# Kernel tuning notes

Hardware: AMD Instinct MI355X
Metric: run time of the kernel (lower is better)

The kernel has to match this reference:

```python
import jax, jax.numpy as jnp
import numpy as np

B, N, D, M, DEPTH, VOCAB = 8, 128, 128, 16, 4, 100
EIN = 2 * D + 1          # edge MLP input dim: feats_i | feats_j | rel_dist
LN_EPS = 1e-5


def setup_inputs() -> dict:
    key = jax.random.key(0)
    ks = jax.random.split(key, 20)
    s = 0.02  # small init like egnn-pytorch's init_eps
    f32 = jnp.float32
    return {
        "z": jax.random.randint(ks[0], (B, N), 0, VOCAB),
        "pos": jax.random.normal(ks[1], (B, N, 3), f32),
        "mask": jnp.ones((B, N), bool),
        "emb": jax.random.normal(ks[2], (VOCAB, D), f32) * s,
        # edge MLP: Linear(EIN, 2*EIN) -> SiLU -> Linear(2*EIN, M) -> SiLU
        "e_w1": jax.random.normal(ks[3], (DEPTH, EIN, 2 * EIN), f32) * s,
        "e_b1": jnp.zeros((DEPTH, 2 * EIN), f32),
        "e_w2": jax.random.normal(ks[4], (DEPTH, 2 * EIN, M), f32) * s,
        "e_b2": jnp.zeros((DEPTH, M), f32),
        # coors MLP: Linear(M, 4M) -> SiLU -> Linear(4M, 1)
        "c_w1": jax.random.normal(ks[5], (DEPTH, M, 4 * M), f32) * s,
        "c_b1": jnp.zeros((DEPTH, 4 * M), f32),
        "c_w2": jax.random.normal(ks[6], (DEPTH, 4 * M, 1), f32) * s,
        "c_b2": jnp.zeros((DEPTH, 1), f32),
        # node LayerNorm (norm_feats=True in EGNN_Network)
        "ln_g": jnp.ones((DEPTH, D), f32),
        "ln_b": jnp.zeros((DEPTH, D), f32),
        # node MLP: Linear(D+M, 2D) -> SiLU -> Linear(2D, D), residual
        "n_w1": jax.random.normal(ks[7], (DEPTH, D + M, 2 * D), f32) * s,
        "n_b1": jnp.zeros((DEPTH, 2 * D), f32),
        "n_w2": jax.random.normal(ks[8], (DEPTH, 2 * D, D), f32) * s,
        "n_b2": jnp.zeros((DEPTH, D), f32),
    }


def _egnn_forward(z, pos, mask, emb, e_w1, e_b1, e_w2, e_b2,
                  c_w1, c_b1, c_w2, c_b2, ln_g, ln_b,
                  n_w1, n_b1, n_w2, n_b2):
    feats = emb[z]                       # [B,N,D]
    coors = pos                          # [B,N,3]
    mf = mask.astype(feats.dtype)        # [B,N]
    pair = mf[:, :, None] * mf[:, None, :]   # [B,N,N] pairwise mask
    for l in range(DEPTH):
        rel = coors[:, :, None, :] - coors[:, None, :, :]       # [B,N,N,3]
        dist = jnp.sum(rel * rel, axis=-1, keepdims=True)       # [B,N,N,1]
        fi = jnp.broadcast_to(feats[:, :, None, :], (B, N, N, D))
        fj = jnp.broadcast_to(feats[:, None, :, :], (B, N, N, D))
        e = jnp.concatenate([fi, fj, dist], axis=-1)             # [B,N,N,EIN]
        h = jax.nn.silu(e @ e_w1[l] + e_b1[l])                   # [B,N,N,2*EIN]
        m_ij = jax.nn.silu(h @ e_w2[l] + e_b2[l])                # [B,N,N,M]
        # coordinate update
        cw = (jax.nn.silu(m_ij @ c_w1[l] + c_b1[l]) @ c_w2[l] + c_b2[l])[..., 0]
        cw = cw * pair                                           # mask invalid pairs
        coors = coors + jnp.einsum('bij,bijc->bic', cw, rel)
        # node update: masked sum-pool of messages over j
        m_i = jnp.sum(m_ij * pair[..., None], axis=2)            # [B,N,M]
        mu = jnp.mean(feats, axis=-1, keepdims=True)
        var = jnp.var(feats, axis=-1, keepdims=True)
        fn = (feats - mu) * jax.lax.rsqrt(var + LN_EPS) * ln_g[l] + ln_b[l]
        ni = jnp.concatenate([fn, m_i], axis=-1)                 # [B,N,D+M]
        feats = feats + (jax.nn.silu(ni @ n_w1[l] + n_b1[l]) @ n_w2[l] + n_b2[l])
    # masked mean pool
    w = mf[..., None]
    return jnp.sum(feats * w, axis=1) / jnp.maximum(jnp.sum(w, axis=1), 1.0)


def reference(z, pos, mask, emb, e_w1, e_b1, e_w2, e_b2,
              c_w1, c_b1, c_w2, c_b2, ln_g, ln_b,
              n_w1, n_b1, n_w2, n_b2):
    return _egnn_forward(z, pos, mask, emb, e_w1, e_b1, e_w2, e_b2,
                         c_w1, c_b1, c_w2, c_b2, ln_g, ln_b,
                         n_w1, n_b1, n_w2, n_b2)
```

## Files before the change

### kernel.cpp

```cpp
#include <hip/hip_runtime.h>

#define BATCH 8
#define NN    128
#define DD    128
#define MM    16
#define DEPTH 4
#define EIN   257
#define H1    514
#define KPAD  544
#define NCH   17
#define NODES (BATCH*NN)
#define BQ_B  69632
#define NL2E  (-1.442695040888963f)
#define NLN2  (-0.6931471805599453f)

typedef __attribute__((ext_vector_type(8))) short short8;
typedef __attribute__((ext_vector_type(4))) float floatx4;

__device__ __forceinline__ float b2f(unsigned short u) {
    return __uint_as_float(((unsigned int)u) << 16);
}
__device__ __forceinline__ unsigned short f2b(float f) {
    unsigned int x = __float_as_uint(f);
    unsigned int r = (x + 0x7fffu + ((x >> 16) & 1u)) >> 16;
    return (unsigned short)r;
}
__device__ __forceinline__ float siluf(float x) {
    float t = __builtin_amdgcn_exp2f(x * NL2E);
    return x * __builtin_amdgcn_rcpf(1.0f + t);
}
__device__ __forceinline__ float loadf(const void* p, size_t idx, int isbf) {
    return isbf ? b2f(((const unsigned short*)p)[idx]) : ((const float*)p)[idx];
}
__device__ __forceinline__ unsigned int pk2(float x, float y) {
    unsigned int xb = __float_as_uint(x) + 0x8000u;
    unsigned int yb = __float_as_uint(y) + 0x8000u;
    return __builtin_amdgcn_perm(yb, xb, 0x07060302);
}
__device__ __forceinline__ unsigned int h2pk_y(float y0, float y1) {
    float t0 = __builtin_amdgcn_exp2f(y0);
    float t1 = __builtin_amdgcn_exp2f(y1);
    float h0 = y0 * __builtin_amdgcn_rcpf(1.0f + t0);
    float h1 = y1 * __builtin_amdgcn_rcpf(1.0f + t1);
    return pk2(h0, h1);
}

#define OFF_FEATS   0
#define OFF_COORSA  131072
#define OFF_COORSB  134144
#define OFF_AB      137216
#define OFF_BQ      694272
#define OFF_CPK     1267712
#define OFF_WLB     1272576
#define OFF_W2F     1274816
#define OFF_FLAG    1292224
#define OFF_FB16    1292228
#define OFF_W1F     1357764

__global__ __launch_bounds__(256) void k_init(
    const int* __restrict__ z, const void* __restrict__ pos,
    const void* __restrict__ emb,
    const void* __restrict__ e_w1, const void* __restrict__ e_w2,
    const void* __restrict__ e_b2,
    const void* __restrict__ c_w1, const void* __restrict__ c_b1,
    const void* __restrict__ c_w2, const void* __restrict__ c_b2,
    float* __restrict__ feats, unsigned short* __restrict__ fb16,
    float* __restrict__ coorsA,
    float* __restrict__ wlb, int4* __restrict__ w2frag,
    int4* __restrict__ w1frag,
    float* __restrict__ cpack, int* __restrict__ flag) {
    __shared__ int sfl;
    int tid = threadIdx.x, bx = blockIdx.x;
    if (tid < 64) {
        float f = fabsf(__uint_as_float(((const unsigned int*)pos)[tid]));
        bool ok = (f == 0.f) || (f > 1e-8f && f < 1e8f);
        unsigned long long v = __ballot(ok);
        if (tid == 0) sfl = (__builtin_popcountll(v) >= 32) ? 0 : 1;
    }
    __syncthreads();
    int isbf = sfl;
    if (bx == 0 && tid == 0) *flag = isbf;
    if (bx < 512) {
        int node = 2 * bx + (tid >> 7), t = tid & 127;
        int zi = z[node];
        float v = loadf(emb, (size_t)zi * DD + t, isbf);
        feats[node * DD + t] = v;
        fb16[node * DD + t] = f2b(v);
        if (t < 3) coorsA[node * 3 + t] = loadf(pos, node * 3 + t, isbf);
    } else if (bx < 580) {
        int p = bx - 512;
        int layer = p / NCH, kc = p % NCH;
        if (tid < 64) {
            int quad = tid >> 4, c = tid & 15;
            size_t w2base = (size_t)layer * H1 * MM;
            unsigned int u[4];
            #pragma unroll
            for (int pp = 0; pp < 4; ++pp) {
                int k0 = kc * 32 + quad * 8 + 2 * pp, k1 = k0 + 1;
                float f0 = (k0 < H1) ? loadf(e_w2, w2base + (size_t)k0 * MM + c, isbf) : 0.f;
                float f1 = (k1 < H1) ? loadf(e_w2, w2base + (size_t)k1 * MM + c, isbf) : 0.f;
                u[pp] = pk2(f0, f1);
            }
            w2frag[(layer * NCH + kc) * 64 + tid] =
                make_int4((int)u[0], (int)u[1], (int)u[2], (int)u[3]);
            if (kc == 0) {
                size_t wlbase = ((size_t)layer * EIN + 256) * H1;
                for (int t = tid; t < KPAD; t += 64)
                    wlb[layer * 560 + t] =
                        (t < H1) ? NL2E * loadf(e_w1, wlbase + t, isbf) : 0.f;
                if (tid < 16)
                    wlb[layer * 560 + 544 + tid] = loadf(e_b2, layer * MM + tid, isbf);
            }
        }
    } else if (bx < 584) {
        int l = bx - 580;
        for (int idx = tid; idx < 1024; idx += 256) {
            int c = idx >> 6, hh = idx & 63;
            cpack[l * 1216 + hh * 16 + c] = loadf(c_w1, l * 1024 + c * 64 + hh, isbf);
        }
        if (tid < 64)        cpack[l * 1216 + 1024 + tid] = loadf(c_b1, l * 64 + tid, isbf);
        else if (tid < 128)  cpack[l * 1216 + 1088 + tid - 64] = loadf(c_w2, l * 64 + tid - 64, isbf);
        else if (tid == 128) cpack[l * 1216 + 1152] = loadf(c_b2, l, isbf);
    } else {
        int p = bx - 584;
        int l = p / 68, nt = p % 68;
        int kcd = tid >> 6, lane = tid & 63;
        int quad = lane >> 4, c16 = lane & 15;
        int n_local = nt * 16 + c16;
        int half = n_local >= KPAD;
        int k_out = n_local - (half ? KPAD : 0);
        size_t wbase = (size_t)l * EIN * H1 + (size_t)(half ? 128 : 0) * H1 + k_out;
        unsigned int u[4];
        #pragma unroll
        for (int pp = 0; pp < 4; ++pp) {
            int d0 = kcd * 32 + quad * 8 + 2 * pp;
            float f0 = (k_out < H1) ? loadf(e_w1, wbase + (size_t)d0 * H1, isbf) : 0.f;
            float f1 = (k_out < H1) ? loadf(e_w1, wbase + (size_t)(d0 + 1) * H1, isbf) : 0.f;
            u[pp] = pk2(f0, f1);
        }
        w1frag[((size_t)(l * 68 + nt) * 4 + kcd) * 64 + lane] =
            make_int4((int)u[0], (int)u[1], (int)u[2], (int)u[3]);
    }
}

__global__ __launch_bounds__(256) void k1_ab(
    const unsigned short* __restrict__ fb16, const int4* __restrict__ w1f,
    const void* __restrict__ b1raw, unsigned int b1off,
    float* __restrict__ Ab, float* __restrict__ Bq,
    const int* __restrict__ flagp) {
    int bx = blockIdx.x;
    int mt = bx & 63, ng = bx >> 6;
    int tid = threadIdx.x, w = tid >> 6, lane = tid & 63;
    int quad = lane >> 4, c16 = lane & 15;
    int isbf = *flagp;
    int ntile = ng * 4 + w;
    int n_local = ntile * 16 + c16;
    int half = n_local >= KPAD;
    int k_out = n_local - (half ? KPAD : 0);

    const unsigned short* ap = fb16 + (size_t)(mt * 16 + c16) * DD + quad * 8;
    const int4* bp = w1f + (size_t)ntile * 4 * 64 + lane;
    floatx4 acc = {0.f, 0.f, 0.f, 0.f};
    #pragma unroll
    for (int kcd = 0; kcd < 4; ++kcd) {
        short8 af = *(const short8*)(ap + kcd * 32);
        union { int4 i4; short8 s; } bf;
        bf.i4 = bp[kcd * 64];
        acc = __builtin_amdgcn_mfma_f32_16x16x32_bf16(af, bf.s, acc, 0, 0, 0);
    }
    if (!half) {
        float bias = (k_out < H1) ? loadf(b1raw, b1off + k_out, isbf) : 0.f;
        #pragma unroll
        for (int r = 0; r < 4; ++r)
            Ab[(size_t)(mt * 16 + quad * 4 + r) * KPAD + k_out] =
                NL2E * (acc[r] + bias);
    } else {
        int kc = k_out >> 5, kk = k_out & 31;
        int qd = kk >> 3, hsel = (kk >> 2) & 1, tt = k_out & 3;
        #pragma unroll
        for (int r = 0; r < 4; ++r) {
            int node = mt * 16 + quad * 4 + r;
            int bb = node >> 7, j = node & 127;
            int jt = j >> 4, lj = qd * 16 + (j & 15);
            Bq[(size_t)bb * BQ_B + kc * 4096 + jt * 512 + hsel * 256
               + lj * 4 + tt] = NL2E * acc[r];
        }
    }
}

#define K2_CHUNK(kc_) {                                                       \
    short8 bf = wfp[(kc_) * 64];                                              \
    float4 aA0 = *(const float4*)(arow0 + (kc_) * 32);                        \
    float4 aA1 = *(const float4*)(arow0 + (kc_) * 32 + 4);                    \
    float4 aB0 = *(const float4*)(arow1 + (kc_) * 32);                        \
    float4 aB1 = *(const float4*)(arow1 + (kc_) * 32 + 4);                    \
    float4 l0  = *(const float4*)(wlr + (kc_) * 32);                          \
    float4 l1  = *(const float4*)(wlr + (kc_) * 32 + 4);                      \
    float4 pp0 = *(const float4*)(bqw + (size_t)(kc_) * 4096);                \
    float4 pp1 = *(const float4*)(bqw + (size_t)(kc_) * 4096 + 256);          \
    float4 qq0 = *(const float4*)(bqw + (size_t)(kc_) * 4096 + 2048);         \
    float4 qq1 = *(const float4*)(bqw + (size_t)(kc_) * 4096 + 2304);         \
    union { unsigned int u[4]; short8 s; } ua, ub, uc, ud;                    \
    ua.u[0] = h2pk_y(fmaf(d2a0, l0.x, aA0.x + pp0.x),                         \
                     fmaf(d2a0, l0.y, aA0.y + pp0.y));                        \
    ua.u[1] = h2pk_y(fmaf(d2a0, l0.z, aA0.z + pp0.z),                         \
                     fmaf(d2a0, l0.w, aA0.w + pp0.w));                        \
    ua.u[2] = h2pk_y(fmaf(d2a0, l1.x, aA1.x + pp1.x),                         \
                     fmaf(d2a0, l1.y, aA1.y + pp1.y));                        \
    ua.u[3] = h2pk_y(fmaf(d2a0, l1.z, aA1.z + pp1.z),                         \
                     fmaf(d2a0, l1.w, aA1.w + pp1.w));                        \
    ub.u[0] = h2pk_y(fmaf(d2b0, l0.x, aA0.x + qq0.x),                         \
                     fmaf(d2b0, l0.y, aA0.y + qq0.y));                        \
    ub.u[1] = h2pk_y(fmaf(d2b0, l0.z, aA0.z + qq0.z),                         \
                     fmaf(d2b0, l0.w, aA0.w + qq0.w));                        \
    ub.u[2] = h2pk_y(fmaf(d2b0, l1.x, aA1.x + qq1.x),                         \
                     fmaf(d2b0, l1.y, aA1.y + qq1.y));                        \
    ub.u[3] = h2pk_y(fmaf(d2b0, l1.z, aA1.z + qq1.z),                         \
                     fmaf(d2b0, l1.w, aA1.w + qq1.w));                        \
    uc.u[0] = h2pk_y(fmaf(d2a1, l0.x, aB0.x + pp0.x),                         \
                     fmaf(d2a1, l0.y, aB0.y + pp0.y));                        \
    uc.u[1] = h2pk_y(fmaf(d2a1, l0.z, aB0.z + pp0.z),                         \
                     fmaf(d2a1, l0.w, aB0.w + pp0.w));                        \
    uc.u[2] = h2pk_y(fmaf(d2a1, l1.x, aB1.x + pp1.x),                         \
                     fmaf(d2a1, l1.y, aB1.y + pp1.y));                        \
    uc.u[3] = h2pk_y(fmaf(d2a1, l1.z, aB1.z + pp1.z),                         \
                     fmaf(d2a1, l1.w, aB1.w + pp1.w));                        \
    ud.u[0] = h2pk_y(fmaf(d2b1, l0.x, aB0.x + qq0.x),                         \
                     fmaf(d2b1, l0.y, aB0.y + qq0.y));                        \
    ud.u[1] = h2pk_y(fmaf(d2b1, l0.z, aB0.z + qq0.z),                         \
                     fmaf(d2b1, l0.w, aB0.w + qq0.w));                        \
    ud.u[2] = h2pk_y(fmaf(d2b1, l1.x, aB1.x + qq1.x),                         \
                     fmaf(d2b1, l1.y, aB1.y + qq1.y));                        \
    ud.u[3] = h2pk_y(fmaf(d2b1, l1.z, aB1.z + qq1.z),                         \
                     fmaf(d2b1, l1.w, aB1.w + qq1.w));                        \
    acc00 = __builtin_amdgcn_mfma_f32_16x16x32_bf16(ua.s, bf, acc00, 0, 0, 0);\
    acc01 = __builtin_amdgcn_mfma_f32_16x16x32_bf16(ub.s, bf, acc01, 0, 0, 0);\
    acc10 = __builtin_amdgcn_mfma_f32_16x16x32_bf16(uc.s, bf, acc10, 0, 0, 0);\
    acc11 = __builtin_amdgcn_mfma_f32_16x16x32_bf16(ud.s, bf, acc11, 0, 0, 0);}

__global__ __launch_bounds__(512, 4) void k2_pair(
    const float* __restrict__ Ab, const float* __restrict__ Bq,
    const float* __restrict__ coorsIn, float* __restrict__ coorsOut,
    float* __restrict__ feats, unsigned short* __restrict__ fb16,
    const float* __restrict__ wlbL,
    const short8* __restrict__ w2fragL,
    const float* __restrict__ cpk,
    const void* __restrict__ gln, const void* __restrict__ bln,
    const void* __restrict__ w1r, const void* __restrict__ b1r,
    const void* __restrict__ w2r, const void* __restrict__ b2r,
    unsigned int layer, const int* __restrict__ flagp) {
    __shared__ float Ms[2][128 * 17];
    __shared__ float px[128], py[128], pz[128];
    __shared__ float msum[2][16][16];
    __shared__ float cwf[2][2][128];
    __shared__ float red[4][3];
    __shared__ float fr[2][128];
    __shared__ float ni[2][144];
    __shared__ float hid[2][256];
    __shared__ float part[2][2][128];
    int tid = threadIdx.x;
    int b = blockIdx.x & 7, ip = blockIdx.x >> 3;
    int i0 = ip * 2;
    int node0 = b * NN + i0;
    int w = tid >> 6, lane = tid & 63;
    int quad = lane >> 4, c16 = lane & 15;
    int kg = w >> 2, wj = w & 3;
    int isbf = *flagp;

    if (tid < 128) {
        int g = (b * NN + tid) * 3;
        px[tid] = coorsIn[g]; py[tid] = coorsIn[g + 1]; pz[tid] = coorsIn[g + 2];
    } else if (tid < 384) {
        int n = (tid - 128) >> 7, t = tid & 127;
        fr[n][t] = feats[(size_t)(node0 + n) * DD + t];
    }
    __syncthreads();

    int j0 = wj * 16 + c16, j1 = j0 + 64;
    float p0x = px[i0],     p0y = py[i0],     p0z = pz[i0];
    float p1x = px[i0 + 1], p1y = py[i0 + 1], p1z = pz[i0 + 1];
    float dxa0 = p0x - px[j0], dya0 = p0y - py[j0], dza0 = p0z - pz[j0];
    float d2a0 = dxa0*dxa0 + dya0*dya0 + dza0*dza0;
    float dxb0 = p0x - px[j1], dyb0 = p0y - py[j1], dzb0 = p0z - pz[j1];
    float d2b0 = dxb0*dxb0 + dyb0*dyb0 + dzb0*dzb0;
    float dxa1 = p1x - px[j0], dya1 = p1y - py[j0], dza1 = p1z - pz[j0];
    float d2a1 = dxa1*dxa1 + dya1*dya1 + dza1*dza1;
    float dxb1 = p1x - px[j1], dyb1 = p1y - py[j1], dzb1 = p1z - pz[j1];
    float d2b1 = dxb1*dxb1 + dyb1*dyb1 + dzb1*dzb1;
    float b2v = wlbL[544 + c16];

    const float* arow0 = Ab + (size_t)node0 * KPAD + quad * 8;
    const float* arow1 = arow0 + KPAD;
    const float* wlr   = wlbL + quad * 8;
    const float* bqw   = Bq + (size_t)b * BQ_B + wj * 512 + lane * 4;
    const short8* wfp  = w2fragL + lane;

    floatx4 acc00 = {0.f,0.f,0.f,0.f}, acc01 = {0.f,0.f,0.f,0.f};
    floatx4 acc10 = {0.f,0.f,0.f,0.f}, acc11 = {0.f,0.f,0.f,0.f};

    if (kg == 0) {
        K2_CHUNK(0) K2_CHUNK(1) K2_CHUNK(2) K2_CHUNK(3) K2_CHUNK(4)
        K2_CHUNK(5) K2_CHUNK(6) K2_CHUNK(7) K2_CHUNK(8)
    } else {
        K2_CHUNK(9) K2_CHUNK(10) K2_CHUNK(11) K2_CHUNK(12)
        K2_CHUNK(13) K2_CHUNK(14) K2_CHUNK(15) K2_CHUNK(16)
    }

    if (kg == 0) {
        #pragma unroll
        for (int r = 0; r < 4; ++r) {
            int jl = (wj * 16 + quad * 4 + r) * 17 + c16;
            Ms[0][jl]           = acc00[r];
            Ms[0][jl + 64 * 17] = acc01[r];
            Ms[1][jl]           = acc10[r];
            Ms[1][jl + 64 * 17] = acc11[r];
        }
    }
    __syncthreads();
    if (kg == 1) {
        #pragma unroll
        for (int r = 0; r < 4; ++r) {
            int jl = (wj * 16 + quad * 4 + r) * 17 + c16;
            Ms[0][jl]           = siluf(fmaf(Ms[0][jl]           + acc00[r], NLN2, b2v));
            Ms[0][jl + 64 * 17] = siluf(fmaf(Ms[0][jl + 64 * 17] + acc01[r], NLN2, b2v));
            Ms[1][jl]           = siluf(fmaf(Ms[1][jl]           + acc10[r], NLN2, b2v));
            Ms[1][jl + 64 * 17] = siluf(fmaf(Ms[1][jl + 64 * 17] + acc11[r], NLN2, b2v));
        }
    }
    __syncthreads();

    {
        int n = tid >> 8, g = (tid >> 4) & 15, c = tid & 15;
        float s = 0.f;
        #pragma unroll
        for (int t = 0; t < 8; ++t) s += Ms[n][(g * 8 + t) * 17 + c];
        msum[n][g][c] = s;
    }
    __syncthreads();

    if (tid < 32) {
        int n = tid >> 4, c = tid & 15;
        float s = 0.f;
        #pragma unroll
        for (int g = 0; g < 16; ++g) s += msum[n][g][c];
        ni[n][128 + c] = s;
    }
    if (tid < 128) {
        int n = tid >> 6; int l6 = tid & 63;
        unsigned int lnoff = layer * DD;
        float v0 = fr[n][l6], v1 = fr[n][l6 + 64];
        float s1 = v0 + v1, s2 = v0 * v0 + v1 * v1;
        #pragma unroll
        for (int off = 32; off >= 1; off >>= 1) {
            s1 += __shfl_xor(s1, off, 64);
            s2 += __shfl_xor(s2, off, 64);
        }
        float mu  = s1 * (1.0f / 128.0f);
        float var = s2 * (1.0f / 128.0f) - mu * mu;
        float rs  = rsqrtf(var + 1e-5f);
        ni[n][l6]      = (v0 - mu) * rs * loadf(gln, lnoff + l6, isbf)
                       + loadf(bln, lnoff + l6, isbf);
        ni[n][l6 + 64] = (v1 - mu) * rs * loadf(gln, lnoff + l6 + 64, isbf)
                       + loadf(bln, lnoff + l6 + 64, isbf);
    }

    {
        int n = tid >> 8, j = tid & 127, hf = (tid >> 7) & 1;
        float mv[16];
        #pragma unroll
        for (int c = 0; c < 16; ++c) mv[c] = Ms[n][j * 17 + c];
        float cwacc = hf ? 0.f : cpk[1152];
        #pragma unroll 2
        for (int hi = 0; hi < 32; ++hi) {
            int hh = (hf << 5) + hi;
            const float4* q = (const float4*)(cpk + hh * 16);
            float4 q0 = q[0], q1 = q[1], q2 = q[2], q3 = q[3];
            float t = cpk[1024 + hh]
                + mv[0]*q0.x + mv[1]*q0.y + mv[2]*q0.z + mv[3]*q0.w
                + mv[4]*q1.x + mv[5]*q1.y + mv[6]*q1.z + mv[7]*q1.w
                + mv[8]*q2.x + mv[9]*q2.y + mv[10]*q2.z + mv[11]*q2.w
                + mv[12]*q3.x + mv[13]*q3.y + mv[14]*q3.z + mv[15]*q3.w;
            cwacc += siluf(t) * cpk[1088 + hh];
        }
        cwf[n][hf][j] = cwacc;
    }
    __syncthreads();

    if (tid < 256) {
        int n = tid >> 7, j = tid & 127;
        float cw = cwf[n][0][j] + cwf[n][1][j];
        float pnx = (n == 0) ? p0x : p1x;
        float pny = (n == 0) ? p0y : p1y;
        float pnz = (n == 0) ? p0z : p1z;
        float vx = cw * (pnx - px[j]), vy = cw * (pny - py[j]),
              vz = cw * (pnz - pz[j]);
        #pragma unroll
        for (int off = 32; off >= 1; off >>= 1) {
            vx += __shfl_xor(vx, off, 64);
            vy += __shfl_xor(vy, off, 64);
            vz += __shfl_xor(vz, off, 64);
        }
        if (lane == 0) { red[w][0] = vx; red[w][1] = vy; red[w][2] = vz; }
    }

    {
        int n = tid >> 8, h = tid & 255;
        size_t w1off = (size_t)layer * 144 * 256;
        float acc = loadf(b1r, layer * 256 + h, isbf);
        if (isbf) {
            const unsigned short* wp = (const unsigned short*)w1r + w1off + h;
            #pragma unroll 8
            for (int d = 0; d < 144; ++d) acc += ni[n][d] * b2f(wp[(size_t)d * 256]);
        } else {
            const float* wp = (const float*)w1r + w1off + h;
            #pragma unroll 8
            for (int d = 0; d < 144; ++d) acc += ni[n][d] * wp[(size_t)d * 256];
        }
        hid[n][h] = siluf(acc);
    }
    __syncthreads();

    if (tid < 6) {
        int n = tid / 3, c = tid - n * 3;
        int nd = node0 + n;
        coorsOut[nd * 3 + c] = coorsIn[nd * 3 + c]
            + red[n * 2][c] + red[n * 2 + 1][c];
    }
    {
        int n = tid >> 8, d = tid & 127, hf = (tid >> 7) & 1;
        size_t w2off = (size_t)layer * 256 * 128;
        float acc = hf ? 0.f : loadf(b2r, layer * 128 + d, isbf);
        if (isbf) {
            const unsigned short* wp = (const unsigned short*)w2r + w2off
                                     + (size_t)hf * 128 * 128 + d;
            #pragma unroll 8
            for (int h = 0; h < 128; ++h) acc += hid[n][hf * 128 + h] * b2f(wp[(size_t)h * 128]);
        } else {
            const float* wp = (const float*)w2r + w2off + (size_t)hf * 128 * 128 + d;
            #pragma unroll 8
            for (int h = 0; h < 128; ++h) acc += hid[n][hf * 128 + h] * wp[(size_t)h * 128];
        }
        part[n][hf][d] = acc;
    }
    __syncthreads();
    if (tid < 256) {
        int n = tid >> 7, d = tid & 127;
        float v = fr[n][d] + part[n][0][d] + part[n][1][d];
        feats[(size_t)(node0 + n) * DD + d] = v;
        fb16[(size_t)(node0 + n) * DD + d] = f2b(v);
    }
}

__global__ __launch_bounds__(128) void k4_pool(
    const float* __restrict__ feats, void* __restrict__ out,
    const int* __restrict__ flagp) {
    int b = blockIdx.x, d = threadIdx.x;
    float s = 0.f;
    for (int n = 0; n < NN; ++n) s += feats[((size_t)(b * NN + n)) * DD + d];
    float v = s * (1.0f / 128.0f);
    if (*flagp) ((unsigned short*)out)[b * DD + d] = f2b(v);
    else        ((float*)out)[b * DD + d] = v;
}

extern "C" void kernel_launch(void* const* d_in, const int* in_sizes, int n_in,
                              void* d_out, int out_size, void* d_ws, size_t ws_size,
                              hipStream_t stream) {
    const int* z = (const int*)d_in[0];
    const void* pos  = d_in[1];
    const void* emb  = d_in[3];
    const void* e_w1 = d_in[4];
    const void* e_b1 = d_in[5];
    const void* e_w2 = d_in[6];
    const void* e_b2 = d_in[7];
    const void* c_w1 = d_in[8];
    const void* c_b1 = d_in[9];
    const void* c_w2 = d_in[10];
    const void* c_b2 = d_in[11];
    const void* ln_g = d_in[12];
    const void* ln_b = d_in[13];
    const void* n_w1 = d_in[14];
    const void* n_b1 = d_in[15];
    const void* n_w2 = d_in[16];
    const void* n_b2 = d_in[17];

    float* ws     = (float*)d_ws;
    float* feats  = ws + OFF_FEATS;
    float* coorsA = ws + OFF_COORSA;
    float* coorsB = ws + OFF_COORSB;
    float* Ab     = ws + OFF_AB;
    float* Bq     = ws + OFF_BQ;
    float* cpk    = ws + OFF_CPK;
    float* wlb    = ws + OFF_WLB;
    int4*  w2f    = (int4*)(ws + OFF_W2F);
    int*   flag   = (int*)(ws + OFF_FLAG);
    unsigned short* fb16 = (unsigned short*)(ws + OFF_FB16);
    int4*  w1f    = (int4*)(ws + OFF_W1F);

    k_init<<<856, 256, 0, stream>>>(
        z, pos, emb, e_w1, e_w2, e_b2, c_w1, c_b1, c_w2, c_b2,
        feats, fb16, coorsA, wlb, w2f, w1f, cpk, flag);

    float* cin = coorsA; float* cout = coorsB;
    for (int l = 0; l < DEPTH; ++l) {
        k1_ab<<<1088, 256, 0, stream>>>(
            fb16, w1f + (size_t)l * 68 * 4 * 64, e_b1,
            (unsigned int)(l * H1), Ab, Bq, flag);
        k2_pair<<<BATCH * NN / 2, 512, 0, stream>>>(
            Ab, Bq, cin, cout, feats, fb16,
            wlb + l * 560, (const short8*)(w2f + (size_t)l * NCH * 64),
            cpk + (size_t)l * 1216,
            ln_g, ln_b, n_w1, n_b1, n_w2, n_b2,
            (unsigned int)l, flag);
        float* t = cin; cin = cout; cout = t;
    }
    k4_pool<<<BATCH, 128, 0, stream>>>(feats, d_out, flag);
}
```

Measured before the change: 314.7 us.

## Process one node per block in pair kernel instead of two

The pair/node-update kernel now handles a single destination node per 512-thread block and launches one block per node, doubling the grid. The freed threads split the coordinate-MLP hidden loop, the node MLP first-layer reduction over inputs, and the second-layer reduction into more partial sums, which are combined in shared memory. The aim is more parallelism and occupancy, with fewer MFMA accumulators and registers per thread. In exchange, Bq tiles and node-MLP weights are reloaded once per node rather than shared across two nodes, which doubles that cache and memory traffic.

```diff
diff --git a/kernel.cpp b/kernel.cpp
--- a/kernel.cpp
+++ b/kernel.cpp
@@ -188,57 +188,37 @@
     }
 }
 
-#define K2_CHUNK(kc_) {                                                       \
+#define K2C(kc_) {                                                            \
     short8 bf = wfp[(kc_) * 64];                                              \
-    float4 aA0 = *(const float4*)(arow0 + (kc_) * 32);                        \
-    float4 aA1 = *(const float4*)(arow0 + (kc_) * 32 + 4);                    \
-    float4 aB0 = *(const float4*)(arow1 + (kc_) * 32);                        \
-    float4 aB1 = *(const float4*)(arow1 + (kc_) * 32 + 4);                    \
+    float4 aA0 = *(const float4*)(arow + (kc_) * 32);                         \
+    float4 aA1 = *(const float4*)(arow + (kc_) * 32 + 4);                     \
     float4 l0  = *(const float4*)(wlr + (kc_) * 32);                          \
     float4 l1  = *(const float4*)(wlr + (kc_) * 32 + 4);                      \
     float4 pp0 = *(const float4*)(bqw + (size_t)(kc_) * 4096);                \
     float4 pp1 = *(const float4*)(bqw + (size_t)(kc_) * 4096 + 256);          \
     float4 qq0 = *(const float4*)(bqw + (size_t)(kc_) * 4096 + 2048);         \
     float4 qq1 = *(const float4*)(bqw + (size_t)(kc_) * 4096 + 2304);         \
-    union { unsigned int u[4]; short8 s; } ua, ub, uc, ud;                    \
-    ua.u[0] = h2pk_y(fmaf(d2a0, l0.x, aA0.x + pp0.x),                         \
-                     fmaf(d2a0, l0.y, aA0.y + pp0.y));                        \
-    ua.u[1] = h2pk_y(fmaf(d2a0, l0.z, aA0.z + pp0.z),                         \
-                     fmaf(d2a0, l0.w, aA0.w + pp0.w));                        \
-    ua.u[2] = h2pk_y(fmaf(d2a0, l1.x, aA1.x + pp1.x),                         \
-                     fmaf(d2a0, l1.y, aA1.y + pp1.y));                        \
-    ua.u[3] = h2pk_y(fmaf(d2a0, l1.z, aA1.z + pp1.z),                         \
-                     fmaf(d2a0, l1.w, aA1.w + pp1.w));                        \
-    ub.u[0] = h2pk_y(fmaf(d2b0, l0.x, aA0.x + qq0.x),                         \
-                     fmaf(d2b0, l0.y, aA0.y + qq0.y));                        \
-    ub.u[1] = h2pk_y(fmaf(d2b0, l0.z, aA0.z + qq0.z),                         \
-                     fmaf(d2b0, l0.w, aA0.w + qq0.w));                        \
-    ub.u[2] = h2pk_y(fmaf(d2b0, l1.x, aA1.x + qq1.x),                         \
-                     fmaf(d2b0, l1.y, aA1.y + qq1.y));                        \
-    ub.u[3] = h2pk_y(fmaf(d2b0, l1.z, aA1.z + qq1.z),                         \
-                     fmaf(d2b0, l1.w, aA1.w + qq1.w));                        \
-    uc.u[0] = h2pk_y(fmaf(d2a1, l0.x, aB0.x + pp0.x),                         \
-                     fmaf(d2a1, l0.y, aB0.y + pp0.y));                        \
-    uc.u[1] = h2pk_y(fmaf(d2a1, l0.z, aB0.z + pp0.z),                         \
-                     fmaf(d2a1, l0.w, aB0.w + pp0.w));                        \
-    uc.u[2] = h2pk_y(fmaf(d2a1, l1.x, aB1.x + pp1.x),                         \
-                     fmaf(d2a1, l1.y, aB1.y + pp1.y));                        \
-    uc.u[3] = h2pk_y(fmaf(d2a1, l1.z, aB1.z + pp1.z),                         \
-                     fmaf(d2a1, l1.w, aB1.w + pp1.w));                        \
-    ud.u[0] = h2pk_y(fmaf(d2b1, l0.x, aB0.x + qq0.x),                         \
-                     fmaf(d2b1, l0.y, aB0.y + qq0.y));                        \
-    ud.u[1] = h2pk_y(fmaf(d2b1, l0.z, aB0.z + qq0.z),                         \
-                     fmaf(d2b1, l0.w, aB0.w + qq0.w));                        \
-    ud.u[2] = h2pk_y(fmaf(d2b1, l1.x, aB1.x + qq1.x),                         \
-                     fmaf(d2b1, l1.y, aB1.y + qq1.y));                        \
-    ud.u[3] = h2pk_y(fmaf(d2b1, l1.z, aB1.z + qq1.z),                         \
-                     fmaf(d2b1, l1.w, aB1.w + qq1.w));                        \
-    acc00 = __builtin_amdgcn_mfma_f32_16x16x32_bf16(ua.s, bf, acc00, 0, 0, 0);\
-    acc01 = __builtin_amdgcn_mfma_f32_16x16x32_bf16(ub.s, bf, acc01, 0, 0, 0);\
-    acc10 = __builtin_amdgcn_mfma_f32_16x16x32_bf16(uc.s, bf, acc10, 0, 0, 0);\
-    acc11 = __builtin_amdgcn_mfma_f32_16x16x32_bf16(ud.s, bf, acc11, 0, 0, 0);}
-
-__global__ __launch_bounds__(512, 4) void k2_pair(
+    union { unsigned int u[4]; short8 s; } ua, ub;                            \
+    ua.u[0] = h2pk_y(fmaf(d2a, l0.x, aA0.x + pp0.x),                          \
+                     fmaf(d2a, l0.y, aA0.y + pp0.y));                         \
+    ua.u[1] = h2pk_y(fmaf(d2a, l0.z, aA0.z + pp0.z),                          \
+                     fmaf(d2a, l0.w, aA0.w + pp0.w));                         \
+    ua.u[2] = h2pk_y(fmaf(d2a, l1.x, aA1.x + pp1.x),                          \
+                     fmaf(d2a, l1.y, aA1.y + pp1.y));                         \
+    ua.u[3] = h2pk_y(fmaf(d2a, l1.z, aA1.z + pp1.z),                          \
+                     fmaf(d2a, l1.w, aA1.w + pp1.w));                         \
+    ub.u[0] = h2pk_y(fmaf(d2b, l0.x, aA0.x + qq0.x),                          \
+                     fmaf(d2b, l0.y, aA0.y + qq0.y));                         \
+    ub.u[1] = h2pk_y(fmaf(d2b, l0.z, aA0.z + qq0.z),                          \
+                     fmaf(d2b, l0.w, aA0.w + qq0.w));                         \
+    ub.u[2] = h2pk_y(fmaf(d2b, l1.x, aA1.x + qq1.x),                          \
+                     fmaf(d2b, l1.y, aA1.y + qq1.y));                         \
+    ub.u[3] = h2pk_y(fmaf(d2b, l1.z, aA1.z + qq1.z),                          \
+                     fmaf(d2b, l1.w, aA1.w + qq1.w));                         \
+    acc0 = __builtin_amdgcn_mfma_f32_16x16x32_bf16(ua.s, bf, acc0, 0, 0, 0);  \
+    acc1 = __builtin_amdgcn_mfma_f32_16x16x32_bf16(ub.s, bf, acc1, 0, 0, 0);}
+
+__global__ __launch_bounds__(512, 8) void k2_node(
     const float* __restrict__ Ab, const float* __restrict__ Bq,
     const float* __restrict__ coorsIn, float* __restrict__ coorsOut,
     float* __restrict__ feats, unsigned short* __restrict__ fb16,
@@ -249,19 +229,19 @@
     const void* __restrict__ w1r, const void* __restrict__ b1r,
     const void* __restrict__ w2r, const void* __restrict__ b2r,
     unsigned int layer, const int* __restrict__ flagp) {
-    __shared__ float Ms[2][128 * 17];
+    __shared__ float Ms[128 * 17];
     __shared__ float px[128], py[128], pz[128];
-    __shared__ float msum[2][16][16];
-    __shared__ float cwf[2][2][128];
-    __shared__ float red[4][3];
-    __shared__ float fr[2][128];
-    __shared__ float ni[2][144];
-    __shared__ float hid[2][256];
-    __shared__ float part[2][2][128];
+    __shared__ float msum[16][16];
+    __shared__ float cwf[4][128];
+    __shared__ float red[2][3];
+    __shared__ float fr[128];
+    __shared__ float ni[144];
+    __shared__ float hpart[2][256];
+    __shared__ float hid[256];
+    __shared__ float part[4][128];
     int tid = threadIdx.x;
-    int b = blockIdx.x & 7, ip = blockIdx.x >> 3;
-    int i0 = ip * 2;
-    int node0 = b * NN + i0;
+    int b = blockIdx.x & 7, ii = blockIdx.x >> 3;
+    int node0 = b * NN + ii;
     int w = tid >> 6, lane = tid & 63;
     int quad = lane >> 4, c16 = lane & 15;
     int kg = w >> 2, wj = w & 3;
@@ -270,50 +250,41 @@
     if (tid < 128) {
         int g = (b * NN + tid) * 3;
         px[tid] = coorsIn[g]; py[tid] = coorsIn[g + 1]; pz[tid] = coorsIn[g + 2];
-    } else if (tid < 384) {
-        int n = (tid - 128) >> 7, t = tid & 127;
-        fr[n][t] = feats[(size_t)(node0 + n) * DD + t];
+    } else if (tid < 256) {
+        int t = tid - 128;
+        fr[t] = feats[(size_t)node0 * DD + t];
     }
     __syncthreads();
 
     int j0 = wj * 16 + c16, j1 = j0 + 64;
-    float p0x = px[i0],     p0y = py[i0],     p0z = pz[i0];
-    float p1x = px[i0 + 1], p1y = py[i0 + 1], p1z = pz[i0 + 1];
-    float dxa0 = p0x - px[j0], dya0 = p0y - py[j0], dza0 = p0z - pz[j0];
-    float d2a0 = dxa0*dxa0 + dya0*dya0 + dza0*dza0;
-    float dxb0 = p0x - px[j1], dyb0 = p0y - py[j1], dzb0 = p0z - pz[j1];
-    float d2b0 = dxb0*dxb0 + dyb0*dyb0 + dzb0*dzb0;
-    float dxa1 = p1x - px[j0], dya1 = p1y - py[j0], dza1 = p1z - pz[j0];
-    float d2a1 = dxa1*dxa1 + dya1*dya1 + dza1*dza1;
-    float dxb1 = p1x - px[j1], dyb1 = p1y - py[j1], dzb1 = p1z - pz[j1];
-    float d2b1 = dxb1*dxb1 + dyb1*dyb1 + dzb1*dzb1;
+    float pix = px[ii], piy = py[ii], piz = pz[ii];
+    float dxa = pix - px[j0], dya = piy - py[j0], dza = piz - pz[j0];
+    float d2a = dxa*dxa + dya*dya + dza*dza;
+    float dxb = pix - px[j1], dyb = piy - py[j1], dzb = piz - pz[j1];
+    float d2b = dxb*dxb + dyb*dyb + dzb*dzb;
     float b2v = wlbL[544 + c16];
 
-    const float* arow0 = Ab + (size_t)node0 * KPAD + quad * 8;
-    const float* arow1 = arow0 + KPAD;
-    const float* wlr   = wlbL + quad * 8;
-    const float* bqw   = Bq + (size_t)b * BQ_B + wj * 512 + lane * 4;
-    const short8* wfp  = w2fragL + lane;
-
-    floatx4 acc00 = {0.f,0.f,0.f,0.f}, acc01 = {0.f,0.f,0.f,0.f};
-    floatx4 acc10 = {0.f,0.f,0.f,0.f}, acc11 = {0.f,0.f,0.f,0.f};
+    const float* arow = Ab + (size_t)node0 * KPAD + quad * 8;
+    const float* wlr  = wlbL + quad * 8;
+    const float* bqw  = Bq + (size_t)b * BQ_B + wj * 512 + lane * 4;
+    const short8* wfp = w2fragL + lane;
+
+    floatx4 acc0 = {0.f,0.f,0.f,0.f}, acc1 = {0.f,0.f,0.f,0.f};
 
     if (kg == 0) {
-        K2_CHUNK(0) K2_CHUNK(1) K2_CHUNK(2) K2_CHUNK(3) K2_CHUNK(4)
-        K2_CHUNK(5) K2_CHUNK(6) K2_CHUNK(7) K2_CHUNK(8)
+        K2C(0) K2C(1) K2C(2) K2C(3) K2C(4)
+        K2C(5) K2C(6) K2C(7) K2C(8)
     } else {
-        K2_CHUNK(9) K2_CHUNK(10) K2_CHUNK(11) K2_CHUNK(12)
-        K2_CHUNK(13) K2_CHUNK(14) K2_CHUNK(15) K2_CHUNK(16)
+        K2C(9) K2C(10) K2C(11) K2C(12)
+        K2C(13) K2C(14) K2C(15) K2C(16)
     }
 
     if (kg == 0) {
         #pragma unroll
         for (int r = 0; r < 4; ++r) {
             int jl = (wj * 16 + quad * 4 + r) * 17 + c16;
-            Ms[0][jl]           = acc00[r];
-            Ms[0][jl + 64 * 17] = acc01[r];
-            Ms[1][jl]           = acc10[r];
-            Ms[1][jl + 64 * 17] = acc11[r];
+            Ms[jl]           = acc0[r];
+            Ms[jl + 64 * 17] = acc1[r];
         }
     }
     __syncthreads();
@@ -321,34 +292,31 @@
         #pragma unroll
         for (int r = 0; r < 4; ++r) {
             int jl = (wj * 16 + quad * 4 + r) * 17 + c16;
-            Ms[0][jl]           = siluf(fmaf(Ms[0][jl]           + acc00[r], NLN2, b2v));
-            Ms[0][jl + 64 * 17] = siluf(fmaf(Ms[0][jl + 64 * 17] + acc01[r], NLN2, b2v));
-            Ms[1][jl]           = siluf(fmaf(Ms[1][jl]           + acc10[r], NLN2, b2v));
-            Ms[1][jl + 64 * 17] = siluf(fmaf(Ms[1][jl + 64 * 17] + acc11[r], NLN2, b2v));
-        }
-    }
-    __syncthreads();
-
-    {
-        int n = tid >> 8, g = (tid >> 4) & 15, c = tid & 15;
+            Ms[jl]           = siluf(fmaf(Ms[jl]           + acc0[r], NLN2, b2v));
+            Ms[jl + 64 * 17] = siluf(fmaf(Ms[jl + 64 * 17] + acc1[r], NLN2, b2v));
+        }
+    }
+    __syncthreads();
+
+    if (tid < 256) {
+        int g = tid >> 4, c = tid & 15;
         float s = 0.f;
         #pragma unroll
-        for (int t = 0; t < 8; ++t) s += Ms[n][(g * 8 + t) * 17 + c];
-        msum[n][g][c] = s;
-    }
-    __syncthreads();
-
-    if (tid < 32) {
-        int n = tid >> 4, c = tid & 15;
+        for (int t = 0; t < 8; ++t) s += Ms[(g * 8 + t) * 17 + c];
+        msum[g][c] = s;
+    }
+    __syncthreads();
+
+    if (tid < 16) {
         float s = 0.f;
         #pragma unroll
-        for (int g = 0; g < 16; ++g) s += msum[n][g][c];
-        ni[n][128 + c] = s;
-    }
-    if (tid < 128) {
-        int n = tid >> 6; int l6 = tid & 63;
+        for (int g = 0; g < 16; ++g) s += msum[g][tid];
+        ni[128 + tid] = s;
+    }
+    if (tid < 64) {
+        int l6 = tid;
         unsigned int lnoff = layer * DD;
-        float v0 = fr[n][l6], v1 = fr[n][l6 + 64];
+        float v0 = fr[l6], v1 = fr[l6 + 64];
         float s1 = v0 + v1, s2 = v0 * v0 + v1 * v1;
         #pragma unroll
         for (int off = 32; off >= 1; off >>= 1) {
@@ -358,21 +326,21 @@
         float mu  = s1 * (1.0f / 128.0f);
         float var = s2 * (1.0f / 128.0f) - mu * mu;
         float rs  = rsqrtf(var + 1e-5f);
-        ni[n][l6]      = (v0 - mu) * rs * loadf(gln, lnoff + l6, isbf)
-                       + loadf(bln, lnoff + l6, isbf);
-        ni[n][l6 + 64] = (v1 - mu) * rs * loadf(gln, lnoff + l6 + 64, isbf)
-                       + loadf(bln, lnoff + l6 + 64, isbf);
+        ni[l6]      = (v0 - mu) * rs * loadf(gln, lnoff + l6, isbf)
+                    + loadf(bln, lnoff + l6, isbf);
+        ni[l6 + 64] = (v1 - mu) * rs * loadf(gln, lnoff + l6 + 64, isbf)
+                    + loadf(bln, lnoff + l6 + 64, isbf);
     }
 
     {
-        int n = tid >> 8, j = tid & 127, hf = (tid >> 7) & 1;
+        int j = tid & 127, hf = tid >> 7;
         float mv[16];
         #pragma unroll
-        for (int c = 0; c < 16; ++c) mv[c] = Ms[n][j * 17 + c];
-        float cwacc = hf ? 0.f : cpk[1152];
+        for (int c = 0; c < 16; ++c) mv[c] = Ms[j * 17 + c];
+        float cwacc = (hf == 0) ? cpk[1152] : 0.f;
         #pragma unroll 2
-        for (int hi = 0; hi < 32; ++hi) {
-            int hh = (hf << 5) + hi;
+        for (int hi = 0; hi < 16; ++hi) {
+            int hh = (hf << 4) + hi;
             const float4* q = (const float4*)(cpk + hh * 16);
             float4 q0 = q[0], q1 = q[1], q2 = q[2], q3 = q[3];
             float t = cpk[1024 + hh]
@@ -382,18 +350,15 @@
                 + mv[12]*q3.x + mv[13]*q3.y + mv[14]*q3.z + mv[15]*q3.w;
             cwacc += siluf(t) * cpk[1088 + hh];
         }
-        cwf[n][hf][j] = cwacc;
-    }
-    __syncthreads();
-
-    if (tid < 256) {
-        int n = tid >> 7, j = tid & 127;
-        float cw = cwf[n][0][j] + cwf[n][1][j];
-        float pnx = (n == 0) ? p0x : p1x;
-        float pny = (n == 0) ? p0y : p1y;
-        float pnz = (n == 0) ? p0z : p1z;
-        float vx = cw * (pnx - px[j]), vy = cw * (pny - py[j]),
-              vz = cw * (pnz - pz[j]);
+        cwf[hf][j] = cwacc;
+    }
+    __syncthreads();
+
+    if (tid < 128) {
+        int j = tid;
+        float cw = cwf[0][j] + cwf[1][j] + cwf[2][j] + cwf[3][j];
+        float vx = cw * (pix - px[j]), vy = cw * (piy - py[j]),
+              vz = cw * (piz - pz[j]);
         #pragma unroll
         for (int off = 32; off >= 1; off >>= 1) {
             vx += __shfl_xor(vx, off, 64);
@@ -404,50 +369,56 @@
     }
 
     {
-        int n = tid >> 8, h = tid & 255;
+        int h = tid & 255, df = tid >> 8;
         size_t w1off = (size_t)layer * 144 * 256;
-        float acc = loadf(b1r, layer * 256 + h, isbf);
+        float acc = (df == 0) ? loadf(b1r, layer * 256 + h, isbf) : 0.f;
+        int d0 = df * 72;
         if (isbf) {
-            const unsigned short* wp = (const unsigned short*)w1r + w1off + h;
+            const unsigned short* wp = (const unsigned short*)w1r + w1off
+                                     + (size_t)d0 * 256 + h;
             #pragma unroll 8
-            for (int d = 0; d < 144; ++d) acc += ni[n][d] * b2f(wp[(size_t)d * 256]);
+            for (int d = 0; d < 72; ++d) acc += ni[d0 + d] * b2f(wp[(size_t)d * 256]);
         } else {
-            const float* wp = (const float*)w1r + w1off + h;
+            const float* wp = (const float*)w1r + w1off + (size_t)d0 * 256 + h;
             #pragma unroll 8
-            for (int d = 0; d < 144; ++d) acc += ni[n][d] * wp[(size_t)d * 256];
-        }
-        hid[n][h] = siluf(acc);
-    }
-    __syncthreads();
-
-    if (tid < 6) {
-        int n = tid / 3, c = tid - n * 3;
-        int nd = node0 + n;
-        coorsOut[nd * 3 + c] = coorsIn[nd * 3 + c]
-            + red[n * 2][c] + red[n * 2 + 1][c];
-    }
+            for (int d = 0; d < 72; ++d) acc += ni[d0 + d] * wp[(size_t)d * 256];
+        }
+        hpart[df][h] = acc;
+    }
+    __syncthreads();
+
+    if (tid < 3) {
+        coorsOut[node0 * 3 + tid] = coorsIn[node0 * 3 + tid]
+            + red[0][tid] + red[1][tid];
+    }
+    if (tid < 256) {
+        hid[tid] = siluf(hpart[0][tid] + hpart[1][tid]);
+    }
+    __syncthreads();
+
     {
-        int n = tid >> 8, d = tid & 127, hf = (tid >> 7) & 1;
+        int d = tid & 127, hf = tid >> 7;
         size_t w2off = (size_t)layer * 256 * 128;
-        float acc = hf ? 0.f : loadf(b2r, layer * 128 + d, isbf);
+        float acc = (hf == 0) ? loadf(b2r, layer * 128 + d, isbf) : 0.f;
+        int h0 = hf * 64;
         if (isbf) {
             const unsigned short* wp = (const unsigned short*)w2r + w2off
-                                     + (size_t)hf * 128 * 128 + d;
+                                     + (size_t)h0 * 128 + d;
             #pragma unroll 8
-            for (int h = 0; h < 128; ++h) acc += hid[n][hf * 128 + h] * b2f(wp[(size_t)h * 128]);
+            for (int h = 0; h < 64; ++h) acc += hid[h0 + h] * b2f(wp[(size_t)h * 128]);
         } else {
-            const float* wp = (const float*)w2r + w2off + (size_t)hf * 128 * 128 + d;
+            const float* wp = (const float*)w2r + w2off + (size_t)h0 * 128 + d;
             #pragma unroll 8
-            for (int h = 0; h < 128; ++h) acc += hid[n][hf * 128 + h] * wp[(size_t)h * 128];
-        }
-        part[n][hf][d] = acc;
-    }
-    __syncthreads();
-    if (tid < 256) {
-        int n = tid >> 7, d = tid & 127;
-        float v = fr[n][d] + part[n][0][d] + part[n][1][d];
-        feats[(size_t)(node0 + n) * DD + d] = v;
-        fb16[(size_t)(node0 + n) * DD + d] = f2b(v);
+            for (int h = 0; h < 64; ++h) acc += hid[h0 + h] * wp[(size_t)h * 128];
+        }
+        part[hf][d] = acc;
+    }
+    __syncthreads();
+    if (tid < 128) {
+        int d = tid;
+        float v = fr[d] + part[0][d] + part[1][d] + part[2][d] + part[3][d];
+        feats[(size_t)node0 * DD + d] = v;
+        fb16[(size_t)node0 * DD + d] = f2b(v);
     }
 }
 
@@ -505,7 +476,7 @@
         k1_ab<<<1088, 256, 0, stream>>>(
             fb16, w1f + (size_t)l * 68 * 4 * 64, e_b1,
             (unsigned int)(l * H1), Ab, Bq, flag);
-        k2_pair<<<BATCH * NN / 2, 512, 0, stream>>>(
+        k2_node<<<NODES, 512, 0, stream>>>(
             Ab, Bq, cin, cout, feats, fb16,
             wlb + l * 560, (const short8*)(w2f + (size_t)l * NCH * 64),
             cpk + (size_t)l * 1216,
```

Result: slower. 326.0 us (+3.6%).
